# Performance work log

Measured on AMD Instinct MI355X. Metric: run time of the kernel, lower is better.

## Reference

```python
import jax, jax.numpy as jnp
import numpy as np

N, IN, H, C, E = 20000, 256, 256, 16, 640000

def sage_conv(x, edge_index, W_l, b_l, W_r):
    # PyG SAGEConv (aggr='mean', root_weight=True):
    # out = lin_l(mean_{j in N(i)} x_j) + lin_r(x_i)
    src, dst = edge_index[0], edge_index[1]
    n = x.shape[0]
    msgs = x[src]                                            # [E, d] irregular gather
    agg = jax.ops.segment_sum(msgs, dst, num_segments=n)     # [N, d]
    deg = jax.ops.segment_sum(jnp.ones((msgs.shape[0],), x.dtype), dst, num_segments=n)
    agg = agg / jnp.maximum(deg, 1.0)[:, None]               # mean aggregation
    return agg @ W_l + b_l + x @ W_r


def setup_inputs() -> dict:
    key = jax.random.key(0)
    ks = jax.random.split(key, 10)
    s = lambda k, fi, fo: jax.random.normal(k, (fi, fo), jnp.float32) / np.sqrt(fi)
    return {
        "x": jax.random.normal(ks[0], (N, IN), jnp.float32),
        "edge_index": jax.random.randint(ks[1], (2, E), 0, N, jnp.int64),
        "W1l": s(ks[2], IN, H), "b1": jnp.zeros((H,), jnp.float32), "W1r": s(ks[3], IN, H),
        "W2l": s(ks[4], H, H),  "b2": jnp.zeros((H,), jnp.float32), "W2r": s(ks[5], H, H),
        "Wc": s(ks[6], H, C),   "bc": jnp.zeros((C,), jnp.float32),
    }


def reference(x, edge_index, W1l, b1, W1r, W2l, b2, W2r, Wc, bc):
    h = sage_conv(x, edge_index, W1l, b1, W1r)
    h = jax.nn.relu(h)                    # dropout is identity in eval mode
    z = sage_conv(h, edge_index, W2l, b2, W2r)
    return z @ Wc + bc                    # classifier logits [N, C]
```

## Files before the change

kernel.cpp:

```cpp
#include <hip/hip_runtime.h>
#include <hip/hip_bf16.h>


#define FEAT 256
#define NCLS 16
#define ZPAD 264
#define NSH  8
#define SCAP 64
#define SLOTS (NSH * SCAP)
#define CAPTOT 128

typedef __bf16 bf16x8 __attribute__((ext_vector_type(8)));
typedef __bf16 bf16x4 __attribute__((ext_vector_type(4)));
typedef float  f32x4  __attribute__((ext_vector_type(4)));
typedef float  f32x2  __attribute__((ext_vector_type(2)));
typedef unsigned int uint4v __attribute__((ext_vector_type(4)));

#define ACC8(S, U) do {                                                   \
    _Pragma("unroll")                                                     \
    for (int w_ = 0; w_ < 4; ++w_) {                                      \
        f32x2 lo_ = __builtin_amdgcn_cvt_pk_f32_fp8(U[w_], false);        \
        f32x2 hi_ = __builtin_amdgcn_cvt_pk_f32_fp8(U[w_], true);         \
        S[w_][0] += lo_[0]; S[w_][1] += lo_[1];                           \
        S[w_][2] += hi_[0]; S[w_][3] += hi_[1];                           \
    } } while (0)

__device__ __forceinline__ void load_entries(
    const int* __restrict__ cnt, const unsigned short* __restrict__ bucket,
    int node, int lane, int& e0, int& e1, int& deg, float& inv)
{
    int4 ca = *(const int4*)(cnt + node * NSH);
    int4 cb = *(const int4*)(cnt + node * NSH + 4);
    int cs[NSH] = {ca.x, ca.y, ca.z, ca.w, cb.x, cb.y, cb.z, cb.w};
    int ctrue = 0, d = 0;
    #pragma unroll
    for (int s = 0; s < NSH; ++s) {
        ctrue += cs[s];
        cs[s] = cs[s] < SCAP ? cs[s] : SCAP;
        d += cs[s];
    }
    deg = d < CAPTOT ? d : CAPTOT;
    inv = ctrue > 0 ? 1.0f / (float)ctrue : 0.0f;
    const unsigned short* lst = bucket + (size_t)node * SLOTS;

    auto get = [&](int i) -> int {
        int s = 0, loc = i;
        #pragma unroll
        for (int t = 0; t < NSH - 1; ++t) {
            if (s == t && loc >= cs[t]) { loc -= cs[t]; s = t + 1; }
        }
        return lst[s * SCAP + loc];
    };
    e0 = (lane < deg) ? get(lane) : 0;
    e1 = 0;
    if (deg > 64)
        e1 = (lane + 64 < deg) ? get(lane + 64) : 0;
}


__global__ __launch_bounds__(256) void fill_kernel(
    const int* __restrict__ src, const int* __restrict__ dst,
    int* __restrict__ cnt, unsigned short* __restrict__ bucket, int E)
{
    int sh = blockIdx.x & (NSH - 1);
    int e4 = (blockIdx.x * 256 + threadIdx.x) * 4;
    if (e4 + 3 < E) {
        int4 sv = *(const int4*)(src + e4);
        int4 dv = *(const int4*)(dst + e4);
        int p0 = atomicAdd(&cnt[dv.x * NSH + sh], 1);
        int p1 = atomicAdd(&cnt[dv.y * NSH + sh], 1);
        int p2 = atomicAdd(&cnt[dv.z * NSH + sh], 1);
        int p3 = atomicAdd(&cnt[dv.w * NSH + sh], 1);
        if (p0 < SCAP) bucket[(size_t)dv.x * SLOTS + sh * SCAP + p0] = (unsigned short)sv.x;
        if (p1 < SCAP) bucket[(size_t)dv.y * SLOTS + sh * SCAP + p1] = (unsigned short)sv.y;
        if (p2 < SCAP) bucket[(size_t)dv.z * SLOTS + sh * SCAP + p2] = (unsigned short)sv.z;
        if (p3 < SCAP) bucket[(size_t)dv.w * SLOTS + sh * SCAP + p3] = (unsigned short)sv.w;
    } else {
        for (int k = 0; k < 4 && e4 + k < E; ++k) {
            int s = src[e4 + k], d = dst[e4 + k];
            int p = atomicAdd(&cnt[d * NSH + sh], 1);
            if (p < SCAP) bucket[(size_t)d * SLOTS + sh * SCAP + p] = (unsigned short)s;
        }
    }
}


__global__ void cvt_kernel(const float* __restrict__ x,
                           const float* __restrict__ W1l, const float* __restrict__ W1r,
                           const float* __restrict__ W2l, const float* __restrict__ W2r,
                           const float* __restrict__ Wc, const float* __restrict__ b2,
                           const float* __restrict__ bc,
                           __bf16* __restrict__ xb, unsigned char* __restrict__ x8,
                           __bf16* __restrict__ W1lT, __bf16* __restrict__ W1rT,
                           __bf16* __restrict__ WaT, __bf16* __restrict__ WbT,
                           float* __restrict__ bc2,
                           int n4, int nb_cvt) {
    int t = threadIdx.x;
    int bx = blockIdx.x;
    if (bx < nb_cvt) {
        int i = bx * 256 + t;
        if (i < n4) {
            f32x4 v = ((const f32x4*)x)[i];
            bf16x4 o;
            #pragma unroll
            for (int j = 0; j < 4; ++j) o[j] = (__bf16)v[j];
            ((bf16x4*)xb)[i] = o;
            int pk = 0;
            pk = __builtin_amdgcn_cvt_pk_fp8_f32(v[0], v[1], pk, false);
            pk = __builtin_amdgcn_cvt_pk_fp8_f32(v[2], v[3], pk, true);
            ((int*)x8)[i] = pk;
        }
    } else if (bx < nb_cvt + 512) {
        int b = bx - nb_cvt;
        int w = b >> 8, nn = b & 255;
        const float* W = w ? W1r : W1l;
        __bf16* WT = w ? W1rT : W1lT;
        WT[nn * FEAT + t] = (__bf16)W[t * FEAT + nn];
    } else if (bx < nb_cvt + 512 + 32) {
        int b = bx - nb_cvt - 512;
        int c = b & 15;
        const float* W = (b < 16) ? W2l : W2r;
        __bf16* WT = (b < 16) ? WaT : WbT;
        float s = 0.f;
        #pragma unroll 4
        for (int m = 0; m < FEAT; ++m)
            s += W[t * FEAT + m] * Wc[m * NCLS + c];
        WT[c * FEAT + t] = (__bf16)s;
    } else {
        if (t < NCLS) {
            float s = 0.f;
            for (int k = 0; k < FEAT; ++k) s += b2[k] * Wc[k * NCLS + t];
            bc2[t] = s + bc[t];
        }
    }
}


__global__ __launch_bounds__(256) void agg_fp8_kernel(
    const unsigned char* __restrict__ t8, const int* __restrict__ cnt,
    const unsigned short* __restrict__ bucket, __bf16* __restrict__ out, int n)
{
    int wave = threadIdx.x >> 6;
    int node = blockIdx.x * 4 + wave;
    if (node >= n) return;
    int lane = threadIdx.x & 63;
    int quad = lane >> 4, l16 = lane & 15;

    int e0, e1, deg; float inv;
    load_entries(cnt, bucket, node, lane, e0, e1, deg, inv);

    f32x4 s0[4], s1[4];
    #pragma unroll
    for (int w = 0; w < 4; ++w) { s0[w] = (f32x4){0.f,0.f,0.f,0.f}; s1[w] = (f32x4){0.f,0.f,0.f,0.f}; }

    int nfull = deg >> 2;
    int rem   = deg & 3;
    const unsigned char* base = t8 + l16 * 16;

    int tt = 0;
    for (; tt + 7 < nfull; tt += 8) {
        int jj[8];
        #pragma unroll
        for (int u = 0; u < 8; ++u) {
            int i = (tt + u) * 4 + quad;
            jj[u] = (i < 64) ? __shfl(e0, i) : __shfl(e1, i - 64);
        }
        uint4v uu[8];
        #pragma unroll
        for (int u = 0; u < 8; ++u)
            uu[u] = *(const uint4v*)(base + (size_t)jj[u] * FEAT);
        #pragma unroll
        for (int u = 0; u < 8; ++u) {
            if (u & 1) ACC8(s1, uu[u]); else ACC8(s0, uu[u]);
        }
    }
    for (; tt + 3 < nfull; tt += 4) {
        int i0 = (tt + 0) * 4 + quad, i1 = (tt + 1) * 4 + quad;
        int i2 = (tt + 2) * 4 + quad, i3 = (tt + 3) * 4 + quad;
        int j0 = (i0 < 64) ? __shfl(e0, i0) : __shfl(e1, i0 - 64);
        int j1 = (i1 < 64) ? __shfl(e0, i1) : __shfl(e1, i1 - 64);
        int j2 = (i2 < 64) ? __shfl(e0, i2) : __shfl(e1, i2 - 64);
        int j3 = (i3 < 64) ? __shfl(e0, i3) : __shfl(e1, i3 - 64);
        uint4v u0 = *(const uint4v*)(base + (size_t)j0 * FEAT);
        uint4v u1 = *(const uint4v*)(base + (size_t)j1 * FEAT);
        uint4v u2 = *(const uint4v*)(base + (size_t)j2 * FEAT);
        uint4v u3 = *(const uint4v*)(base + (size_t)j3 * FEAT);
        ACC8(s0, u0); ACC8(s1, u1); ACC8(s0, u2); ACC8(s1, u3);
    }
    for (; tt < nfull; ++tt) {
        int i = tt * 4 + quad;
        int j = (i < 64) ? __shfl(e0, i) : __shfl(e1, i - 64);
        uint4v u = *(const uint4v*)(base + (size_t)j * FEAT);
        ACC8(s0, u);
    }
    if (rem) {
        int i = nfull * 4 + quad;
        int j = (i < 64) ? __shfl(e0, i) : __shfl(e1, i - 64);
        if (quad < rem) {
            uint4v u = *(const uint4v*)(base + (size_t)j * FEAT);
            ACC8(s1, u);
        }
    }

    #pragma unroll
    for (int w = 0; w < 4; ++w)
        #pragma unroll
        for (int j = 0; j < 4; ++j) {
            float v = s0[w][j] + s1[w][j];
            v += __shfl_xor(v, 16, 64);
            v += __shfl_xor(v, 32, 64);
            s0[w][j] = v;
        }

    bf16x4 o;
    #pragma unroll
    for (int j = 0; j < 4; ++j) o[j] = (__bf16)(s0[quad][j] * inv);
    *(bf16x4*)(out + (size_t)node * FEAT + l16 * 16 + quad * 4) = o;
}


__global__ __launch_bounds__(256) void gemm1_kernel(
    const __bf16* __restrict__ A1, const __bf16* __restrict__ A2,
    const __bf16* __restrict__ B1T, const __bf16* __restrict__ B2T,
    const float* __restrict__ bias,
    const __bf16* __restrict__ WaT, const __bf16* __restrict__ WbT,
    const float* __restrict__ bc2,
    __bf16* __restrict__ pb, float* __restrict__ q, int M)
{
    __shared__ __align__(16) __bf16 tile[16][ZPAD];

    int m0   = blockIdx.x * 16;
    int lane = threadIdx.x & 63;
    int wave = threadIdx.x >> 6;
    int l16  = lane & 15, quad = lane >> 4;

    f32x4 acc[4];
    #pragma unroll
    for (int b = 0; b < 4; ++b) acc[b] = (f32x4){0.f, 0.f, 0.f, 0.f};

    int r = m0 + l16;
    int arow = (r < M) ? r : (M - 1);
    int nbase = wave * 64;

    for (int pass = 0; pass < 2; ++pass) {
        const __bf16* A  = pass ? A2 : A1;
        const __bf16* BT = pass ? B2T : B1T;
        #pragma unroll 2
        for (int kk = 0; kk < 8; ++kk) {
            int k0 = kk * 32 + quad * 8;
            bf16x8 af = *(const bf16x8*)(A + (size_t)arow * FEAT + k0);
            bf16x8 bfm[4];
            #pragma unroll
            for (int nt = 0; nt < 4; ++nt)
                bfm[nt] = *(const bf16x8*)(BT + (size_t)(nbase + nt * 16 + l16) * FEAT + k0);
            #pragma unroll
            for (int nt = 0; nt < 4; ++nt)
                acc[nt] = __builtin_amdgcn_mfma_f32_16x16x32_bf16(af, bfm[nt], acc[nt], 0, 0, 0);
        }
    }

    #pragma unroll
    for (int nt = 0; nt < 4; ++nt) {
        int col = nbase + nt * 16 + l16;
        float bv = bias[col];
        int lr = quad * 4;
        #pragma unroll
        for (int rr = 0; rr < 4; ++rr) {
            float v = acc[nt][rr] + bv;
            tile[lr + rr][col] = (__bf16)(v > 0.f ? v : 0.f);
        }
    }
    __syncthreads();

    if (wave < 2) {
        const __bf16* WT = wave ? WbT : WaT;
        f32x4 a = {0.f, 0.f, 0.f, 0.f};
        #pragma unroll
        for (int kk = 0; kk < 8; ++kk) {
            int k0 = kk * 32 + quad * 8;
            bf16x8 av = *(const bf16x8*)(&tile[l16][k0]);
            bf16x8 bv = *(const bf16x8*)(WT + (size_t)l16 * FEAT + k0);
            a = __builtin_amdgcn_mfma_f32_16x16x32_bf16(av, bv, a, 0, 0, 0);
        }
        if (wave) {
            float qv = bc2[l16];
            #pragma unroll
            for (int rr = 0; rr < 4; ++rr) {
                int row = m0 + quad * 4 + rr;
                if (row < M) q[(size_t)row * NCLS + l16] = a[rr] + qv;
            }
        } else {
            #pragma unroll
            for (int rr = 0; rr < 4; ++rr) {
                int row = m0 + quad * 4 + rr;
                if (row < M) pb[(size_t)row * NCLS + l16] = (__bf16)a[rr];
            }
        }
    }
}


__global__ __launch_bounds__(256) void agg_out_kernel(
    const __bf16* __restrict__ pb, const float* __restrict__ q,
    const int* __restrict__ cnt, const unsigned short* __restrict__ bucket,
    float* __restrict__ out, int n)
{
    int wave = threadIdx.x >> 6;
    int node = blockIdx.x * 4 + wave;
    if (node >= n) return;
    int lane = threadIdx.x & 63;
    int slot = lane >> 2, fq = lane & 3;

    int e0, e1, deg; float inv;
    load_entries(cnt, bucket, node, lane, e0, e1, deg, inv);

    f32x4 acc = {0.f, 0.f, 0.f, 0.f};
    for (int g = 0; g < deg; g += 32) {
        int i0 = g + slot, i1 = g + 16 + slot;
        int j0 = (i0 < 64) ? __shfl(e0, i0) : __shfl(e1, i0 - 64);
        int j1 = (i1 < 64) ? __shfl(e0, i1) : __shfl(e1, i1 - 64);
        bf16x4 a0 = *(const bf16x4*)(pb + (size_t)j0 * NCLS + fq * 4);
        bf16x4 a1 = *(const bf16x4*)(pb + (size_t)j1 * NCLS + fq * 4);
        float m0 = (i0 < deg) ? 1.f : 0.f;
        float m1 = (i1 < deg) ? 1.f : 0.f;
        #pragma unroll
        for (int k = 0; k < 4; ++k)
            acc[k] += m0 * (float)a0[k] + m1 * (float)a1[k];
    }

    #pragma unroll
    for (int k = 0; k < 4; ++k) {
        float v = acc[k];
        v += __shfl_xor(v, 4, 64);
        v += __shfl_xor(v, 8, 64);
        v += __shfl_xor(v, 16, 64);
        v += __shfl_xor(v, 32, 64);
        acc[k] = v;
    }

    if (slot == 0) {
        f32x4 qv = *(const f32x4*)(q + (size_t)node * NCLS + fq * 4);
        f32x4 o;
        #pragma unroll
        for (int k = 0; k < 4; ++k) o[k] = acc[k] * inv + qv[k];
        *(f32x4*)(out + (size_t)node * NCLS + fq * 4) = o;
    }
}


extern "C" void kernel_launch(void* const* d_in, const int* in_sizes, int n_in,
                              void* d_out, int out_size, void* d_ws, size_t ws_size,
                              hipStream_t stream) {
    const float* x   = (const float*)d_in[0];
    const int*   ei  = (const int*)d_in[1];
    const float* W1l = (const float*)d_in[2];
    const float* b1  = (const float*)d_in[3];
    const float* W1r = (const float*)d_in[4];
    const float* W2l = (const float*)d_in[5];
    const float* b2  = (const float*)d_in[6];
    const float* W2r = (const float*)d_in[7];
    const float* Wc  = (const float*)d_in[8];
    const float* bc  = (const float*)d_in[9];
    float* out = (float*)d_out;

    const int n = in_sizes[0] / FEAT;
    const int E = in_sizes[1] / 2;
    const int* srcp = ei;
    const int* dstp = ei + E;

    char* p = (char*)d_ws;
    auto alloc = [&](size_t bytes) { char* r = p; p += (bytes + 511) & ~511ull; return r; };
    int* cnt       = (int*)alloc((size_t)n * NSH * 4);
    unsigned short* bucket = (unsigned short*)alloc((size_t)n * SLOTS * 2);
    __bf16* W1lT   = (__bf16*)alloc((size_t)FEAT * FEAT * 2);
    __bf16* W1rT   = (__bf16*)alloc((size_t)FEAT * FEAT * 2);
    __bf16* WaT    = (__bf16*)alloc((size_t)NCLS * FEAT * 2);
    __bf16* WbT    = (__bf16*)alloc((size_t)NCLS * FEAT * 2);
    float*  bc2    = (float*)alloc((size_t)NCLS * 4);
    __bf16* xb     = (__bf16*)alloc((size_t)n * FEAT * 2);
    unsigned char* x8 = (unsigned char*)alloc((size_t)n * FEAT);
    __bf16* aggb   = (__bf16*)alloc((size_t)n * FEAT * 2);
    __bf16* pb     = (__bf16*)alloc((size_t)n * NCLS * 2);
    float*  qb     = (float*)alloc((size_t)n * NCLS * 4);

    int n4 = n * FEAT / 4;
    int nb_cvt  = (n4 + 255) / 256;
    int nb_fill = (E + 1023) / 1024;

    hipMemsetAsync(cnt, 0, (size_t)n * NSH * 4, stream);

    fill_kernel<<<nb_fill, 256, 0, stream>>>(srcp, dstp, cnt, bucket, E);

    cvt_kernel<<<nb_cvt + 512 + 32 + 1, 256, 0, stream>>>(
        x, W1l, W1r, W2l, W2r, Wc, b2, bc,
        xb, x8, W1lT, W1rT, WaT, WbT, bc2, n4, nb_cvt);

    agg_fp8_kernel<<<(n + 3) / 4, 256, 0, stream>>>(x8, cnt, bucket, aggb, n);
    gemm1_kernel<<<(n + 15) / 16, 256, 0, stream>>>(aggb, xb, W1lT, W1rT, b1,
                                                    WaT, WbT, bc2, pb, qb, n);

    agg_out_kernel<<<(n + 3) / 4, 256, 0, stream>>>(pb, qb, cnt, bucket, out, n);
}
```

Before: 226.6 us.

## Enlarge gemm1 row tile to 64 and stage A operands in LDS

The fused layer-1 GEMM now covers 64 rows per block instead of 16. Both A inputs (aggregated and raw features) are first staged cooperatively into shared memory, and each wave computes a 4x4 grid of MFMA tiles, so every weight fragment loaded from global memory is reused across four row fragments. The second projection to the 16 classes now uses all four waves instead of two. The cost is a much larger shared-memory footprint (about 67KB) and more accumulator registers, which lowers occupancy and leaves only about 313 blocks.

```diff
diff --git a/kernel.cpp b/kernel.cpp
--- a/kernel.cpp
+++ b/kernel.cpp
@@ -5,6 +5,7 @@
 #define FEAT 256
 #define NCLS 16
 #define ZPAD 264
+#define MT   64
 #define NSH  8
 #define SCAP 64
 #define SLOTS (NSH * SCAP)
@@ -227,73 +228,103 @@
     const float* __restrict__ bc2,
     __bf16* __restrict__ pb, float* __restrict__ q, int M)
 {
-    __shared__ __align__(16) __bf16 tile[16][ZPAD];
-
-    int m0   = blockIdx.x * 16;
-    int lane = threadIdx.x & 63;
-    int wave = threadIdx.x >> 6;
+    __shared__ __align__(16) __bf16 lds[2][MT][ZPAD];
+
+    int m0   = blockIdx.x * MT;
+    int t    = threadIdx.x;
+    int lane = t & 63;
+    int wave = t >> 6;
     int l16  = lane & 15, quad = lane >> 4;
 
-    f32x4 acc[4];
-    #pragma unroll
-    for (int b = 0; b < 4; ++b) acc[b] = (f32x4){0.f, 0.f, 0.f, 0.f};
-
-    int r = m0 + l16;
-    int arow = (r < M) ? r : (M - 1);
+    #pragma unroll 4
+    for (int it = 0; it < 16; ++it) {
+        int i = it * 256 + t;
+        int pass = i >> 11;
+        int r    = (i >> 5) & 63;
+        int c8   = (i & 31) * 8;
+        int gr = m0 + r; gr = (gr < M) ? gr : (M - 1);
+        const __bf16* A = pass ? A2 : A1;
+        *(bf16x8*)(&lds[pass][r][c8]) = *(const bf16x8*)(A + (size_t)gr * FEAT + c8);
+    }
+    __syncthreads();
+
+    f32x4 acc[4][4];
+    #pragma unroll
+    for (int a = 0; a < 4; ++a)
+        #pragma unroll
+        for (int b = 0; b < 4; ++b) acc[a][b] = (f32x4){0.f, 0.f, 0.f, 0.f};
+
     int nbase = wave * 64;
 
+    #pragma unroll 1
     for (int pass = 0; pass < 2; ++pass) {
-        const __bf16* A  = pass ? A2 : A1;
         const __bf16* BT = pass ? B2T : B1T;
         #pragma unroll 2
         for (int kk = 0; kk < 8; ++kk) {
             int k0 = kk * 32 + quad * 8;
-            bf16x8 af = *(const bf16x8*)(A + (size_t)arow * FEAT + k0);
-            bf16x8 bfm[4];
+            bf16x8 af[4], bfm[4];
+            #pragma unroll
+            for (int mf = 0; mf < 4; ++mf)
+                af[mf] = *(const bf16x8*)(&lds[pass][mf * 16 + l16][k0]);
             #pragma unroll
             for (int nt = 0; nt < 4; ++nt)
                 bfm[nt] = *(const bf16x8*)(BT + (size_t)(nbase + nt * 16 + l16) * FEAT + k0);
             #pragma unroll
-            for (int nt = 0; nt < 4; ++nt)
-                acc[nt] = __builtin_amdgcn_mfma_f32_16x16x32_bf16(af, bfm[nt], acc[nt], 0, 0, 0);
-        }
-    }
+            for (int mf = 0; mf < 4; ++mf)
+                #pragma unroll
+                for (int nt = 0; nt < 4; ++nt)
+                    acc[mf][nt] = __builtin_amdgcn_mfma_f32_16x16x32_bf16(
+                        af[mf], bfm[nt], acc[mf][nt], 0, 0, 0);
+        }
+    }
+    __syncthreads();
 
     #pragma unroll
     for (int nt = 0; nt < 4; ++nt) {
         int col = nbase + nt * 16 + l16;
         float bv = bias[col];
-        int lr = quad * 4;
-        #pragma unroll
-        for (int rr = 0; rr < 4; ++rr) {
-            float v = acc[nt][rr] + bv;
-            tile[lr + rr][col] = (__bf16)(v > 0.f ? v : 0.f);
+        #pragma unroll
+        for (int mf = 0; mf < 4; ++mf) {
+            int lr = mf * 16 + quad * 4;
+            #pragma unroll
+            for (int rr = 0; rr < 4; ++rr) {
+                float v = acc[mf][nt][rr] + bv;
+                lds[0][lr + rr][col] = (__bf16)(v > 0.f ? v : 0.f);
+            }
         }
     }
     __syncthreads();
 
-    if (wave < 2) {
-        const __bf16* WT = wave ? WbT : WaT;
-        f32x4 a = {0.f, 0.f, 0.f, 0.f};
-        #pragma unroll
+    {
+        int half = wave >> 1;
+        const __bf16* WT = (wave & 1) ? WbT : WaT;
+        f32x4 a0 = (f32x4){0.f, 0.f, 0.f, 0.f};
+        f32x4 a1 = (f32x4){0.f, 0.f, 0.f, 0.f};
+        #pragma unroll 2
         for (int kk = 0; kk < 8; ++kk) {
             int k0 = kk * 32 + quad * 8;
-            bf16x8 av = *(const bf16x8*)(&tile[l16][k0]);
             bf16x8 bv = *(const bf16x8*)(WT + (size_t)l16 * FEAT + k0);
-            a = __builtin_amdgcn_mfma_f32_16x16x32_bf16(av, bv, a, 0, 0, 0);
-        }
-        if (wave) {
-            float qv = bc2[l16];
-            #pragma unroll
-            for (int rr = 0; rr < 4; ++rr) {
-                int row = m0 + quad * 4 + rr;
-                if (row < M) q[(size_t)row * NCLS + l16] = a[rr] + qv;
-            }
-        } else {
-            #pragma unroll
-            for (int rr = 0; rr < 4; ++rr) {
-                int row = m0 + quad * 4 + rr;
-                if (row < M) pb[(size_t)row * NCLS + l16] = (__bf16)a[rr];
+            bf16x8 av0 = *(const bf16x8*)(&lds[0][half * 32 + l16][k0]);
+            bf16x8 av1 = *(const bf16x8*)(&lds[0][half * 32 + 16 + l16][k0]);
+            a0 = __builtin_amdgcn_mfma_f32_16x16x32_bf16(av0, bv, a0, 0, 0, 0);
+            a1 = __builtin_amdgcn_mfma_f32_16x16x32_bf16(av1, bv, a1, 0, 0, 0);
+        }
+        #pragma unroll
+        for (int mf = 0; mf < 2; ++mf) {
+            f32x4 a = mf ? a1 : a0;
+            if (wave & 1) {
+                float qv = bc2[l16];
+                #pragma unroll
+                for (int rr = 0; rr < 4; ++rr) {
+                    int row = m0 + half * 32 + mf * 16 + quad * 4 + rr;
+                    if (row < M) q[(size_t)row * NCLS + l16] = a[rr] + qv;
+                }
+            } else {
+                #pragma unroll
+                for (int rr = 0; rr < 4; ++rr) {
+                    int row = m0 + half * 32 + mf * 16 + quad * 4 + rr;
+                    if (row < M) pb[(size_t)row * NCLS + l16] = (__bf16)a[rr];
+                }
             }
         }
     }
@@ -396,8 +427,8 @@
         xb, x8, W1lT, W1rT, WaT, WbT, bc2, n4, nb_cvt);
 
     agg_fp8_kernel<<<(n + 3) / 4, 256, 0, stream>>>(x8, cnt, bucket, aggb, n);
-    gemm1_kernel<<<(n + 15) / 16, 256, 0, stream>>>(aggb, xb, W1lT, W1rT, b1,
-                                                    WaT, WbT, bc2, pb, qb, n);
+    gemm1_kernel<<<(n + MT - 1) / MT, 256, 0, stream>>>(aggb, xb, W1lT, W1rT, b1,
+                                                        WaT, WbT, bc2, pb, qb, n);
 
     agg_out_kernel<<<(n + 3) / 4, 256, 0, stream>>>(pb, qb, cnt, bucket, out, n);
 }
```

Measured after the change: 197.0 us. 13.0% less time.
